# Kernel tuning notes

Measured on AMD Instinct MI355X. Metric: run time of the kernel, lower is better.

The kernel has to match this reference:

```python
import jax, jax.numpy as jnp
import numpy as np

N_NODES = 50000
N_EDGES = 800000
D = 128
N_GRAPHS = 64


def setup_inputs() -> dict:
    key = jax.random.key(0)
    ks = jax.random.split(key, 10)
    x = jax.random.normal(ks[0], (N_NODES, D), dtype=jnp.float32)
    edge_weight = jax.random.uniform(ks[1], (N_EDGES,), dtype=jnp.float32)
    W1 = jax.random.normal(ks[2], (D, D), dtype=jnp.float32) / np.sqrt(D)
    b1 = jax.random.normal(ks[3], (D,), dtype=jnp.float32) * 0.01
    W2 = jax.random.normal(ks[4], (D, D), dtype=jnp.float32) / np.sqrt(D)
    b2 = jax.random.normal(ks[5], (D,), dtype=jnp.float32) * 0.01
    Wh = jax.random.normal(ks[6], (D, 1), dtype=jnp.float32) / np.sqrt(D)
    bh = jax.random.normal(ks[7], (1,), dtype=jnp.float32) * 0.01
    edge_index = jax.random.randint(ks[8], (2, N_EDGES), 0, N_NODES, dtype=jnp.int64)
    batch = jnp.sort(jax.random.randint(ks[9], (N_NODES,), 0, N_GRAPHS, dtype=jnp.int64))
    return {"x": x, "edge_weight": edge_weight, "W1": W1, "b1": b1,
            "W2": W2, "b2": b2, "Wh": Wh, "bh": bh,
            "edge_index": edge_index, "batch": batch}


def reference(x, edge_weight, W1, b1, W2, b2, Wh, bh, edge_index, batch):
    N = x.shape[0]
    # --- GCN normalization with self-loops (computed once; shared by layers) ---
    row, col = edge_index[0], edge_index[1]
    loop = jnp.arange(N, dtype=edge_index.dtype)
    row2 = jnp.concatenate([row, loop])   # source nodes
    col2 = jnp.concatenate([col, loop])   # target nodes
    ew2 = jnp.concatenate([edge_weight, jnp.ones((N,), dtype=x.dtype)])
    deg = jax.ops.segment_sum(ew2, col2, num_segments=N)
    dinv = jnp.where(deg > 0, jax.lax.rsqrt(deg), 0.0)
    norm = dinv[row2] * ew2 * dinv[col2]  # [E+N]

    def gcn_conv(h, W, b):
        h = h @ W                                   # [N, D_out]
        msg = norm[:, None] * h[row2]               # gather + scale, [E+N, D_out]
        return jax.ops.segment_sum(msg, col2, num_segments=N) + b

    # dropout is identity in eval mode
    h = jax.nn.relu(gcn_conv(x, W1, b1))
    h = jax.nn.relu(gcn_conv(h, W2, b2))

    # --- global mean pool over graphs ---
    counts = jax.ops.segment_sum(jnp.ones((N,), dtype=h.dtype), batch, num_segments=N_GRAPHS)
    pooled = jax.ops.segment_sum(h, batch, num_segments=N_GRAPHS)
    pooled = pooled / jnp.maximum(counts, 1.0)[:, None]
    return pooled @ Wh + bh
```

## Files before the change

kernel.cpp:

```cpp
#include <hip/hip_runtime.h>
#include <hip/hip_bf16.h>
#include <hip/hip_fp16.h>
#include <hip/hip_fp8.h>

#define N_NODES  50000
#define N_EDGES  800000
#define D        128
#define N_GRAPHS 64
#define CAP      64
#define EW_SCALE 1048576.0f
#define NB_GEMM1 391
#define NB_FILL  3125
#define NB_AGG16 3125
#define PSTR     ((size_t)N_NODES * 64)

typedef _Float16 half8 __attribute__((ext_vector_type(8)));
typedef _Float16 half4 __attribute__((ext_vector_type(4)));
typedef float   float4v __attribute__((ext_vector_type(4)));
typedef float   f32x2   __attribute__((ext_vector_type(2)));

__device__ __forceinline__ float hu2f(unsigned short u) {
    __half_raw hr; hr.x = u;
    return __half2float(__half(hr));
}
__device__ __forceinline__ float fp8_f32(unsigned char u) {
    f32x2 v = __builtin_amdgcn_cvt_pk_f32_fp8((int)u, false);
    return v[0];
}
__device__ __forceinline__ unsigned char f32_fp8(float f) {
    __hip_fp8_e4m3 q(f);
    return (unsigned char)q.__x;
}
__device__ __forceinline__ void unpack_pd(unsigned long long p, int& n, float& dv) {
    int c = (int)(p >> 40);
    n = c < CAP ? c : CAP;
    dv = rsqrtf(1.0f + (float)(p & 0xFFFFFFFFFFULL) * (1.0f / EW_SCALE));
}

__global__ __launch_bounds__(256) void fused_gemm1_fill(const float* __restrict__ X,
                                                        const float* __restrict__ W,
                                                        unsigned char* __restrict__ Y8,
                                                        const int* __restrict__ ei,
                                                        const float* __restrict__ ew,
                                                        unsigned long long* __restrict__ packed,
                                                        unsigned int* __restrict__ bucket) {
    __shared__ _Float16 Xs[128][72];
    __shared__ _Float16 Wt[128][72];

    if (blockIdx.x >= NB_GEMM1) {
        int e = (blockIdx.x - NB_GEMM1) * 256 + threadIdx.x;
        if (e >= N_EDGES) return;
        int r = ei[e];
        int c = ei[N_EDGES + e];
        float w = ew[e];
        unsigned long long add = (1ULL << 40) | (unsigned long long)(unsigned)(w * EW_SCALE + 0.5f);
        unsigned long long old = atomicAdd(&packed[c], add);
        unsigned pos = (unsigned)(old >> 40);
        if (pos < CAP) {
            unsigned short wh = __half_as_ushort(__float2half_rn(w));
            bucket[(size_t)c * CAP + pos] = (unsigned)r | ((unsigned)wh << 16);
        }
        return;
    }

    const int tid  = threadIdx.x;
    const int row0 = blockIdx.x * 128;
    const int wv   = tid >> 6;
    const int lane = tid & 63;
    const int quad = lane >> 4;
    const int l16  = lane & 15;

    float4v acc[8][2] = {};

    for (int kt = 0; kt < 4; kt++) {
        const int kbase = kt * 32;
        {
            int r  = tid >> 1;
            int rr = row0 + r; if (rr >= N_NODES) rr = N_NODES - 1;
            int k0 = (tid & 1) * 16;
            const float4* src = (const float4*)(X + (size_t)rr * 128 + kbase + k0);
#pragma unroll
            for (int i = 0; i < 4; i++) {
                float4 v = src[i];
                half4 hv;
                hv[0] = (_Float16)v.x; hv[1] = (_Float16)v.y;
                hv[2] = (_Float16)v.z; hv[3] = (_Float16)v.w;
                *(half4*)(&Xs[r][k0 + i * 4]) = hv;
            }
        }
        {
            int k  = tid >> 3;
            int c0 = (tid & 7) * 16;
            const float4* src = (const float4*)(W + (size_t)(kbase + k) * 128 + c0);
#pragma unroll
            for (int i = 0; i < 4; i++) {
                float4 v = src[i];
                Wt[c0 + i * 4 + 0][k] = (_Float16)v.x;
                Wt[c0 + i * 4 + 1][k] = (_Float16)v.y;
                Wt[c0 + i * 4 + 2][k] = (_Float16)v.z;
                Wt[c0 + i * 4 + 3][k] = (_Float16)v.w;
            }
        }
        __syncthreads();

        half8 b0 = *(const half8*)(&Wt[wv * 32 + l16][quad * 8]);
        half8 b1f = *(const half8*)(&Wt[wv * 32 + 16 + l16][quad * 8]);
#pragma unroll
        for (int rt = 0; rt < 8; rt++) {
            half8 a = *(const half8*)(&Xs[rt * 16 + l16][quad * 8]);
            acc[rt][0] = __builtin_amdgcn_mfma_f32_16x16x32_f16(a, b0,  acc[rt][0], 0, 0, 0);
            acc[rt][1] = __builtin_amdgcn_mfma_f32_16x16x32_f16(a, b1f, acc[rt][1], 0, 0, 0);
        }
        __syncthreads();
    }
#pragma unroll
    for (int rt = 0; rt < 8; rt++)
#pragma unroll
        for (int ct = 0; ct < 2; ct++)
#pragma unroll
            for (int r = 0; r < 4; r++) {
                int row = row0 + rt * 16 + quad * 4 + r;
                int col = wv * 32 + ct * 16 + l16;
                if (row < N_NODES)
                    Y8[(size_t)(col >> 6) * PSTR + (size_t)row * 64 + (col & 63)] =
                        f32_fp8(acc[rt][ct][r]);
            }
}

__global__ __launch_bounds__(512) void agg1_gemm2_kernel(const unsigned char* __restrict__ x8in,
                                                         const unsigned long long* __restrict__ packed,
                                                         const unsigned int* __restrict__ bucket,
                                                         const float* __restrict__ b1,
                                                         const float* __restrict__ W2,
                                                         unsigned char* __restrict__ x2) {
    __shared__ _Float16 sh1[16][136];
    const int wv   = threadIdx.x >> 6;
    const int lane = threadIdx.x & 63;
    const int node0 = blockIdx.x * 16;

    const int nodeA = node0 + wv * 2;
    const int nodeB = nodeA + 1;
    int nA; float dvA; unpack_pd(packed[nodeA], nA, dvA);
    int nB; float dvB; unpack_pd(packed[nodeB], nB, dvB);

    unsigned pkA = 0u, pkB = 0u;
    if (lane < nA) {
        unsigned eh = bucket[(size_t)nodeA * CAP + lane];
        int src = eh & 0xFFFFu;
        int sn; float sdv; unpack_pd(packed[src], sn, sdv);
        float v = hu2f((unsigned short)(eh >> 16)) * sdv;
        pkA = (unsigned)src | ((unsigned)__half_as_ushort(__float2half_rn(v)) << 16);
    }
    if (lane < nB) {
        unsigned eh = bucket[(size_t)nodeB * CAP + lane];
        int src = eh & 0xFFFFu;
        int sn; float sdv; unpack_pd(packed[src], sn, sdv);
        float v = hu2f((unsigned short)(eh >> 16)) * sdv;
        pkB = (unsigned)src | ((unsigned)__half_as_ushort(__float2half_rn(v)) << 16);
    }
    int pkiA = (int)pkA, pkiB = (int)pkB;
    int nmax = nA > nB ? nA : nB;

    float hA[2], hB[2];
#pragma unroll
    for (int p = 0; p < 2; p++) {
        const unsigned char* pl = x8in + (size_t)p * PSTR;
        float aA = dvA * fp8_f32(pl[(size_t)nodeA * 64 + lane]);
        float aB = dvB * fp8_f32(pl[(size_t)nodeB * 64 + lane]);
        for (int i = 0; i < nmax; i += 8) {
            unsigned av[8], bv[8];
#pragma unroll
            for (int j = 0; j < 8; j++) {
                av[j] = (unsigned)__shfl(pkiA, i + j);
                bv[j] = (unsigned)__shfl(pkiB, i + j);
            }
            unsigned char mA[8], mB[8];
#pragma unroll
            for (int j = 0; j < 8; j++) mA[j] = pl[(size_t)(av[j] & 0xFFFFu) * 64 + lane];
#pragma unroll
            for (int j = 0; j < 8; j++) mB[j] = pl[(size_t)(bv[j] & 0xFFFFu) * 64 + lane];
#pragma unroll
            for (int j = 0; j < 8; j++)
                aA += hu2f((unsigned short)(av[j] >> 16)) * fp8_f32(mA[j]);
#pragma unroll
            for (int j = 0; j < 8; j++)
                aB += hu2f((unsigned short)(bv[j] >> 16)) * fp8_f32(mB[j]);
        }
        float bb = b1[p * 64 + lane];
        hA[p] = fmaxf(dvA * aA + bb, 0.0f);
        hB[p] = fmaxf(dvB * aB + bb, 0.0f);
    }

    sh1[wv * 2][lane]          = (_Float16)hA[0];
    sh1[wv * 2][64 + lane]     = (_Float16)hA[1];
    sh1[wv * 2 + 1][lane]      = (_Float16)hB[0];
    sh1[wv * 2 + 1][64 + lane] = (_Float16)hB[1];
    __syncthreads();

    const int quad = lane >> 4;
    const int l16  = lane & 15;
    float4v acc0 = {};
#pragma unroll
    for (int kc = 0; kc < 4; kc++) {
        const int k0 = kc * 32;
        half8 a = *(const half8*)(&sh1[l16][k0 + quad * 8]);
        const float* wp = W2 + (size_t)(k0 + quad * 8) * 128 + wv * 16 + l16;
        half8 b;
#pragma unroll
        for (int jj = 0; jj < 8; jj++) b[jj] = (_Float16)wp[jj * 128];
        acc0 = __builtin_amdgcn_mfma_f32_16x16x32_f16(a, b, acc0, 0, 0, 0);
    }
    const int col = wv * 16 + l16;
    unsigned char* x2p = x2 + (size_t)(col >> 6) * PSTR + (col & 63);
#pragma unroll
    for (int r = 0; r < 4; r++) {
        int row = node0 + quad * 4 + r;
        int rn; float s;
        unpack_pd(packed[row], rn, s);
        x2p[(size_t)row * 64] = f32_fp8(acc0[r] * s);
    }
}

__global__ __launch_bounds__(256) void agg_head_kernel(const unsigned char* __restrict__ x8,
                                                       const unsigned long long* __restrict__ packed,
                                                       const unsigned int* __restrict__ bucket,
                                                       const float* __restrict__ bias,
                                                       const float* __restrict__ Wh,
                                                       float* __restrict__ nodedot) {
    const int wv   = threadIdx.x >> 6;
    const int lane = threadIdx.x & 63;

    const int nodeA = blockIdx.x * 8 + wv * 2;
    const int nodeB = nodeA + 1;
    int nA; float dvA; unpack_pd(packed[nodeA], nA, dvA);
    int nB; float dvB; unpack_pd(packed[nodeB], nB, dvB);

    unsigned ehA = (lane < nA) ? bucket[(size_t)nodeA * CAP + lane] : 0u;
    unsigned ehB = (lane < nB) ? bucket[(size_t)nodeB * CAP + lane] : 0u;
    int eiA = (int)ehA, eiB = (int)ehB;
    int nmax = nA > nB ? nA : nB;

    float sA = 0.0f, sB = 0.0f;
#pragma unroll
    for (int p = 0; p < 2; p++) {
        const unsigned char* pl = x8 + (size_t)p * PSTR;
        float aA = fp8_f32(pl[(size_t)nodeA * 64 + lane]);
        float aB = fp8_f32(pl[(size_t)nodeB * 64 + lane]);
        for (int i = 0; i < nmax; i += 8) {
            unsigned av[8], bv[8];
#pragma unroll
            for (int j = 0; j < 8; j++) {
                av[j] = (unsigned)__shfl(eiA, i + j);
                bv[j] = (unsigned)__shfl(eiB, i + j);
            }
            unsigned char mA[8], mB[8];
#pragma unroll
            for (int j = 0; j < 8; j++) mA[j] = pl[(size_t)(av[j] & 0xFFFFu) * 64 + lane];
#pragma unroll
            for (int j = 0; j < 8; j++) mB[j] = pl[(size_t)(bv[j] & 0xFFFFu) * 64 + lane];
#pragma unroll
            for (int j = 0; j < 8; j++)
                aA += hu2f((unsigned short)(av[j] >> 16)) * fp8_f32(mA[j]);
#pragma unroll
            for (int j = 0; j < 8; j++)
                aB += hu2f((unsigned short)(bv[j] >> 16)) * fp8_f32(mB[j]);
        }
        float bb = bias[p * 64 + lane];
        float ww = Wh[p * 64 + lane];
        sA += fmaxf(dvA * aA + bb, 0.0f) * ww;
        sB += fmaxf(dvB * aB + bb, 0.0f) * ww;
    }

#pragma unroll
    for (int off = 32; off > 0; off >>= 1) {
        sA += __shfl_down(sA, off, 64);
        sB += __shfl_down(sB, off, 64);
    }
    if (lane == 0) {
        nodedot[nodeA] = sA;
        nodedot[nodeB] = sB;
    }
}

__global__ __launch_bounds__(256) void final2_kernel(const float* __restrict__ nodedot,
                                                     const int* __restrict__ batch,
                                                     const float* __restrict__ bh,
                                                     float* __restrict__ out) {
    __shared__ float red[256];
    int g = blockIdx.x;
    int lo = 0, hi = N_NODES;
    while (lo < hi) { int mid = (lo + hi) >> 1; if (batch[mid] < g) lo = mid + 1; else hi = mid; }
    int a = lo;
    hi = N_NODES;
    while (lo < hi) { int mid = (lo + hi) >> 1; if (batch[mid] < g + 1) lo = mid + 1; else hi = mid; }
    int b = lo;

    float s = 0.0f;
    for (int n = a + threadIdx.x; n < b; n += 256) s += nodedot[n];
    red[threadIdx.x] = s;
    __syncthreads();
#pragma unroll
    for (int off = 128; off > 0; off >>= 1) {
        if (threadIdx.x < off) red[threadIdx.x] += red[threadIdx.x + off];
        __syncthreads();
    }
    if (threadIdx.x == 0)
        out[g] = red[0] / fmaxf((float)(b - a), 1.0f) + bh[0];
}

extern "C" void kernel_launch(void* const* d_in, const int* in_sizes, int n_in,
                              void* d_out, int out_size, void* d_ws, size_t ws_size,
                              hipStream_t stream) {
    const float* x   = (const float*)d_in[0];
    const float* ew  = (const float*)d_in[1];
    const float* W1  = (const float*)d_in[2];
    const float* b1  = (const float*)d_in[3];
    const float* W2  = (const float*)d_in[4];
    const float* b2  = (const float*)d_in[5];
    const float* Wh  = (const float*)d_in[6];
    const float* bh  = (const float*)d_in[7];
    const int*   ei  = (const int*)d_in[8];
    const int*   bat = (const int*)d_in[9];
    float* out = (float*)d_out;

    char* ws = (char*)d_ws;
    unsigned char* bufA8 = (unsigned char*)ws;            ws += (size_t)N_NODES * D;
    unsigned char* bufB8 = (unsigned char*)ws;            ws += (size_t)N_NODES * D;
    ws += 128 - ((size_t)ws & 127);
    unsigned int* bucket = (unsigned int*)ws;             ws += (size_t)N_NODES * CAP * 4;
    unsigned long long* packed = (unsigned long long*)ws; ws += (size_t)N_NODES * 8;
    float*  nodedot = (float*)ws;                         ws += (size_t)N_NODES * 4;

    const int nb_agg8 = N_NODES / 8;

    hipMemsetAsync(packed, 0, (size_t)N_NODES * 8, stream);

    fused_gemm1_fill<<<NB_GEMM1 + NB_FILL, 256, 0, stream>>>(x, W1, bufA8, ei, ew, packed, bucket);

    agg1_gemm2_kernel<<<NB_AGG16, 512, 0, stream>>>(bufA8, packed, bucket, b1, W2, bufB8);

    agg_head_kernel<<<nb_agg8, 256, 0, stream>>>(bufB8, packed, bucket, b2, Wh, nodedot);

    final2_kernel<<<N_GRAPHS, 256, 0, stream>>>(nodedot, bat, bh, out);
}
```

Measured before the change: 231.4 us.

## Split aggregation kernels per feature plane and unfuse GEMM2 into tiled kernel

Both aggregation kernels now split the two 64-wide fp8 feature planes across separate blocks, doubling block count so that each block touches only one plane's gather footprint, which may improve L2 locality. The fused agg1+GEMM2 is split into an aggregation that writes fp16 H1 to global memory and a separate 128-row tiled MFMA GEMM. This removes the per-block reloading and conversion of W2 from fp32. It adds a 12.8MB fp16 round trip plus an extra launch, and the bucket and edge setup work is now duplicated per plane. Bucket reads use nontemporal loads, and the head partial sums are kept per plane and combined in the final kernel.

```diff
diff --git a/kernel.cpp b/kernel.cpp
--- a/kernel.cpp
+++ b/kernel.cpp
@@ -11,7 +11,6 @@
 #define EW_SCALE 1048576.0f
 #define NB_GEMM1 391
 #define NB_FILL  3125
-#define NB_AGG16 3125
 #define PSTR     ((size_t)N_NODES * 64)
 
 typedef _Float16 half8 __attribute__((ext_vector_type(8)));
@@ -127,16 +126,16 @@
             }
 }
 
-__global__ __launch_bounds__(512) void agg1_gemm2_kernel(const unsigned char* __restrict__ x8in,
+__global__ __launch_bounds__(512) void agg1_plane_kernel(const unsigned char* __restrict__ x8in,
                                                          const unsigned long long* __restrict__ packed,
                                                          const unsigned int* __restrict__ bucket,
                                                          const float* __restrict__ b1,
-                                                         const float* __restrict__ W2,
-                                                         unsigned char* __restrict__ x2) {
-    __shared__ _Float16 sh1[16][136];
+                                                         _Float16* __restrict__ h1out) {
+    const int p    = blockIdx.x & 1;
+    const int grp  = blockIdx.x >> 1;
     const int wv   = threadIdx.x >> 6;
     const int lane = threadIdx.x & 63;
-    const int node0 = blockIdx.x * 16;
+    const int node0 = grp * 16;
 
     const int nodeA = node0 + wv * 2;
     const int nodeB = nodeA + 1;
@@ -145,14 +144,14 @@
 
     unsigned pkA = 0u, pkB = 0u;
     if (lane < nA) {
-        unsigned eh = bucket[(size_t)nodeA * CAP + lane];
+        unsigned eh = __builtin_nontemporal_load(&bucket[(size_t)nodeA * CAP + lane]);
         int src = eh & 0xFFFFu;
         int sn; float sdv; unpack_pd(packed[src], sn, sdv);
         float v = hu2f((unsigned short)(eh >> 16)) * sdv;
         pkA = (unsigned)src | ((unsigned)__half_as_ushort(__float2half_rn(v)) << 16);
     }
     if (lane < nB) {
-        unsigned eh = bucket[(size_t)nodeB * CAP + lane];
+        unsigned eh = __builtin_nontemporal_load(&bucket[(size_t)nodeB * CAP + lane]);
         int src = eh & 0xFFFFu;
         int sn; float sdv; unpack_pd(packed[src], sn, sdv);
         float v = hu2f((unsigned short)(eh >> 16)) * sdv;
@@ -161,124 +160,160 @@
     int pkiA = (int)pkA, pkiB = (int)pkB;
     int nmax = nA > nB ? nA : nB;
 
-    float hA[2], hB[2];
-#pragma unroll
-    for (int p = 0; p < 2; p++) {
-        const unsigned char* pl = x8in + (size_t)p * PSTR;
-        float aA = dvA * fp8_f32(pl[(size_t)nodeA * 64 + lane]);
-        float aB = dvB * fp8_f32(pl[(size_t)nodeB * 64 + lane]);
-        for (int i = 0; i < nmax; i += 8) {
-            unsigned av[8], bv[8];
-#pragma unroll
-            for (int j = 0; j < 8; j++) {
-                av[j] = (unsigned)__shfl(pkiA, i + j);
-                bv[j] = (unsigned)__shfl(pkiB, i + j);
-            }
-            unsigned char mA[8], mB[8];
-#pragma unroll
-            for (int j = 0; j < 8; j++) mA[j] = pl[(size_t)(av[j] & 0xFFFFu) * 64 + lane];
-#pragma unroll
-            for (int j = 0; j < 8; j++) mB[j] = pl[(size_t)(bv[j] & 0xFFFFu) * 64 + lane];
-#pragma unroll
-            for (int j = 0; j < 8; j++)
-                aA += hu2f((unsigned short)(av[j] >> 16)) * fp8_f32(mA[j]);
-#pragma unroll
-            for (int j = 0; j < 8; j++)
-                aB += hu2f((unsigned short)(bv[j] >> 16)) * fp8_f32(mB[j]);
-        }
-        float bb = b1[p * 64 + lane];
-        hA[p] = fmaxf(dvA * aA + bb, 0.0f);
-        hB[p] = fmaxf(dvB * aB + bb, 0.0f);
-    }
-
-    sh1[wv * 2][lane]          = (_Float16)hA[0];
-    sh1[wv * 2][64 + lane]     = (_Float16)hA[1];
-    sh1[wv * 2 + 1][lane]      = (_Float16)hB[0];
-    sh1[wv * 2 + 1][64 + lane] = (_Float16)hB[1];
-    __syncthreads();
-
+    const unsigned char* pl = x8in + (size_t)p * PSTR;
+    float aA = dvA * fp8_f32(pl[(size_t)nodeA * 64 + lane]);
+    float aB = dvB * fp8_f32(pl[(size_t)nodeB * 64 + lane]);
+    for (int i = 0; i < nmax; i += 8) {
+        unsigned av[8], bv[8];
+#pragma unroll
+        for (int j = 0; j < 8; j++) {
+            av[j] = (unsigned)__shfl(pkiA, i + j);
+            bv[j] = (unsigned)__shfl(pkiB, i + j);
+        }
+        unsigned char mA[8], mB[8];
+#pragma unroll
+        for (int j = 0; j < 8; j++) mA[j] = pl[(size_t)(av[j] & 0xFFFFu) * 64 + lane];
+#pragma unroll
+        for (int j = 0; j < 8; j++) mB[j] = pl[(size_t)(bv[j] & 0xFFFFu) * 64 + lane];
+#pragma unroll
+        for (int j = 0; j < 8; j++)
+            aA += hu2f((unsigned short)(av[j] >> 16)) * fp8_f32(mA[j]);
+#pragma unroll
+        for (int j = 0; j < 8; j++)
+            aB += hu2f((unsigned short)(bv[j] >> 16)) * fp8_f32(mB[j]);
+    }
+
+    float bb = b1[p * 64 + lane];
+    _Float16 hA = (_Float16)fmaxf(dvA * aA + bb, 0.0f);
+    _Float16 hB = (_Float16)fmaxf(dvB * aB + bb, 0.0f);
+    __builtin_nontemporal_store(hA, &h1out[(size_t)nodeA * 128 + p * 64 + lane]);
+    __builtin_nontemporal_store(hB, &h1out[(size_t)nodeB * 128 + p * 64 + lane]);
+}
+
+__global__ __launch_bounds__(256) void gemm2_kernel(const _Float16* __restrict__ H1,
+                                                    const float* __restrict__ W,
+                                                    const unsigned long long* __restrict__ packed,
+                                                    unsigned char* __restrict__ Y8) {
+    __shared__ _Float16 Xs[128][72];
+    __shared__ _Float16 Wt[128][72];
+
+    const int tid  = threadIdx.x;
+    const int row0 = blockIdx.x * 128;
+    const int wv   = tid >> 6;
+    const int lane = tid & 63;
     const int quad = lane >> 4;
     const int l16  = lane & 15;
-    float4v acc0 = {};
-#pragma unroll
-    for (int kc = 0; kc < 4; kc++) {
-        const int k0 = kc * 32;
-        half8 a = *(const half8*)(&sh1[l16][k0 + quad * 8]);
-        const float* wp = W2 + (size_t)(k0 + quad * 8) * 128 + wv * 16 + l16;
-        half8 b;
-#pragma unroll
-        for (int jj = 0; jj < 8; jj++) b[jj] = (_Float16)wp[jj * 128];
-        acc0 = __builtin_amdgcn_mfma_f32_16x16x32_f16(a, b, acc0, 0, 0, 0);
-    }
-    const int col = wv * 16 + l16;
-    unsigned char* x2p = x2 + (size_t)(col >> 6) * PSTR + (col & 63);
-#pragma unroll
-    for (int r = 0; r < 4; r++) {
-        int row = node0 + quad * 4 + r;
-        int rn; float s;
-        unpack_pd(packed[row], rn, s);
-        x2p[(size_t)row * 64] = f32_fp8(acc0[r] * s);
-    }
-}
-
-__global__ __launch_bounds__(256) void agg_head_kernel(const unsigned char* __restrict__ x8,
-                                                       const unsigned long long* __restrict__ packed,
-                                                       const unsigned int* __restrict__ bucket,
-                                                       const float* __restrict__ bias,
-                                                       const float* __restrict__ Wh,
-                                                       float* __restrict__ nodedot) {
+
+    float4v acc[8][2] = {};
+
+    for (int kt = 0; kt < 4; kt++) {
+        const int kbase = kt * 32;
+        {
+            int r  = tid >> 1;
+            int rr = row0 + r; if (rr >= N_NODES) rr = N_NODES - 1;
+            int k0 = (tid & 1) * 16;
+            const half8* src = (const half8*)(H1 + (size_t)rr * 128 + kbase + k0);
+            *(half8*)(&Xs[r][k0])     = src[0];
+            *(half8*)(&Xs[r][k0 + 8]) = src[1];
+        }
+        {
+            int k  = tid >> 3;
+            int c0 = (tid & 7) * 16;
+            const float4* src = (const float4*)(W + (size_t)(kbase + k) * 128 + c0);
+#pragma unroll
+            for (int i = 0; i < 4; i++) {
+                float4 v = src[i];
+                Wt[c0 + i * 4 + 0][k] = (_Float16)v.x;
+                Wt[c0 + i * 4 + 1][k] = (_Float16)v.y;
+                Wt[c0 + i * 4 + 2][k] = (_Float16)v.z;
+                Wt[c0 + i * 4 + 3][k] = (_Float16)v.w;
+            }
+        }
+        __syncthreads();
+
+        half8 b0 = *(const half8*)(&Wt[wv * 32 + l16][quad * 8]);
+        half8 b1f = *(const half8*)(&Wt[wv * 32 + 16 + l16][quad * 8]);
+#pragma unroll
+        for (int rt = 0; rt < 8; rt++) {
+            half8 a = *(const half8*)(&Xs[rt * 16 + l16][quad * 8]);
+            acc[rt][0] = __builtin_amdgcn_mfma_f32_16x16x32_f16(a, b0,  acc[rt][0], 0, 0, 0);
+            acc[rt][1] = __builtin_amdgcn_mfma_f32_16x16x32_f16(a, b1f, acc[rt][1], 0, 0, 0);
+        }
+        __syncthreads();
+    }
+#pragma unroll
+    for (int rt = 0; rt < 8; rt++)
+#pragma unroll
+        for (int ct = 0; ct < 2; ct++)
+#pragma unroll
+            for (int r = 0; r < 4; r++) {
+                int row = row0 + rt * 16 + quad * 4 + r;
+                int col = wv * 32 + ct * 16 + l16;
+                if (row < N_NODES) {
+                    int rn; float s;
+                    unpack_pd(packed[row], rn, s);
+                    Y8[(size_t)(col >> 6) * PSTR + (size_t)row * 64 + (col & 63)] =
+                        f32_fp8(acc[rt][ct][r] * s);
+                }
+            }
+}
+
+__global__ __launch_bounds__(256) void agg_head_plane(const unsigned char* __restrict__ x8,
+                                                      const unsigned long long* __restrict__ packed,
+                                                      const unsigned int* __restrict__ bucket,
+                                                      const float* __restrict__ bias,
+                                                      const float* __restrict__ Wh,
+                                                      float* __restrict__ nodedot) {
+    const int p    = blockIdx.x & 1;
+    const int grp  = blockIdx.x >> 1;
     const int wv   = threadIdx.x >> 6;
     const int lane = threadIdx.x & 63;
 
-    const int nodeA = blockIdx.x * 8 + wv * 2;
+    const int nodeA = grp * 8 + wv * 2;
     const int nodeB = nodeA + 1;
     int nA; float dvA; unpack_pd(packed[nodeA], nA, dvA);
     int nB; float dvB; unpack_pd(packed[nodeB], nB, dvB);
 
-    unsigned ehA = (lane < nA) ? bucket[(size_t)nodeA * CAP + lane] : 0u;
-    unsigned ehB = (lane < nB) ? bucket[(size_t)nodeB * CAP + lane] : 0u;
+    unsigned ehA = (lane < nA) ? __builtin_nontemporal_load(&bucket[(size_t)nodeA * CAP + lane]) : 0u;
+    unsigned ehB = (lane < nB) ? __builtin_nontemporal_load(&bucket[(size_t)nodeB * CAP + lane]) : 0u;
     int eiA = (int)ehA, eiB = (int)ehB;
     int nmax = nA > nB ? nA : nB;
 
-    float sA = 0.0f, sB = 0.0f;
-#pragma unroll
-    for (int p = 0; p < 2; p++) {
-        const unsigned char* pl = x8 + (size_t)p * PSTR;
-        float aA = fp8_f32(pl[(size_t)nodeA * 64 + lane]);
-        float aB = fp8_f32(pl[(size_t)nodeB * 64 + lane]);
-        for (int i = 0; i < nmax; i += 8) {
-            unsigned av[8], bv[8];
-#pragma unroll
-            for (int j = 0; j < 8; j++) {
-                av[j] = (unsigned)__shfl(eiA, i + j);
-                bv[j] = (unsigned)__shfl(eiB, i + j);
-            }
-            unsigned char mA[8], mB[8];
-#pragma unroll
-            for (int j = 0; j < 8; j++) mA[j] = pl[(size_t)(av[j] & 0xFFFFu) * 64 + lane];
-#pragma unroll
-            for (int j = 0; j < 8; j++) mB[j] = pl[(size_t)(bv[j] & 0xFFFFu) * 64 + lane];
-#pragma unroll
-            for (int j = 0; j < 8; j++)
-                aA += hu2f((unsigned short)(av[j] >> 16)) * fp8_f32(mA[j]);
-#pragma unroll
-            for (int j = 0; j < 8; j++)
-                aB += hu2f((unsigned short)(bv[j] >> 16)) * fp8_f32(mB[j]);
-        }
-        float bb = bias[p * 64 + lane];
-        float ww = Wh[p * 64 + lane];
-        sA += fmaxf(dvA * aA + bb, 0.0f) * ww;
-        sB += fmaxf(dvB * aB + bb, 0.0f) * ww;
-    }
-
+    const unsigned char* pl = x8 + (size_t)p * PSTR;
+    float aA = fp8_f32(pl[(size_t)nodeA * 64 + lane]);
+    float aB = fp8_f32(pl[(size_t)nodeB * 64 + lane]);
+    for (int i = 0; i < nmax; i += 8) {
+        unsigned av[8], bv[8];
+#pragma unroll
+        for (int j = 0; j < 8; j++) {
+            av[j] = (unsigned)__shfl(eiA, i + j);
+            bv[j] = (unsigned)__shfl(eiB, i + j);
+        }
+        unsigned char mA[8], mB[8];
+#pragma unroll
+        for (int j = 0; j < 8; j++) mA[j] = pl[(size_t)(av[j] & 0xFFFFu) * 64 + lane];
+#pragma unroll
+        for (int j = 0; j < 8; j++) mB[j] = pl[(size_t)(bv[j] & 0xFFFFu) * 64 + lane];
+#pragma unroll
+        for (int j = 0; j < 8; j++)
+            aA += hu2f((unsigned short)(av[j] >> 16)) * fp8_f32(mA[j]);
+#pragma unroll
+        for (int j = 0; j < 8; j++)
+            aB += hu2f((unsigned short)(bv[j] >> 16)) * fp8_f32(mB[j]);
+    }
+
+    float bb = bias[p * 64 + lane];
+    float ww = Wh[p * 64 + lane];
+    float sA = fmaxf(dvA * aA + bb, 0.0f) * ww;
+    float sB = fmaxf(dvB * aB + bb, 0.0f) * ww;
 #pragma unroll
     for (int off = 32; off > 0; off >>= 1) {
         sA += __shfl_down(sA, off, 64);
         sB += __shfl_down(sB, off, 64);
     }
     if (lane == 0) {
-        nodedot[nodeA] = sA;
-        nodedot[nodeB] = sB;
+        nodedot[(size_t)p * N_NODES + nodeA] = sA;
+        nodedot[(size_t)p * N_NODES + nodeB] = sB;
     }
 }
 
@@ -296,7 +331,8 @@
     int b = lo;
 
     float s = 0.0f;
-    for (int n = a + threadIdx.x; n < b; n += 256) s += nodedot[n];
+    for (int n = a + threadIdx.x; n < b; n += 256)
+        s += nodedot[n] + nodedot[(size_t)N_NODES + n];
     red[threadIdx.x] = s;
     __syncthreads();
 #pragma unroll
@@ -329,17 +365,18 @@
     ws += 128 - ((size_t)ws & 127);
     unsigned int* bucket = (unsigned int*)ws;             ws += (size_t)N_NODES * CAP * 4;
     unsigned long long* packed = (unsigned long long*)ws; ws += (size_t)N_NODES * 8;
-    float*  nodedot = (float*)ws;                         ws += (size_t)N_NODES * 4;
-
-    const int nb_agg8 = N_NODES / 8;
+    float*  nodedot = (float*)ws;                         ws += (size_t)N_NODES * 2 * 4;
+    _Float16* h1buf = (_Float16*)ws;                      ws += (size_t)N_NODES * D * 2;
 
     hipMemsetAsync(packed, 0, (size_t)N_NODES * 8, stream);
 
     fused_gemm1_fill<<<NB_GEMM1 + NB_FILL, 256, 0, stream>>>(x, W1, bufA8, ei, ew, packed, bucket);
 
-    agg1_gemm2_kernel<<<NB_AGG16, 512, 0, stream>>>(bufA8, packed, bucket, b1, W2, bufB8);
-
-    agg_head_kernel<<<nb_agg8, 256, 0, stream>>>(bufB8, packed, bucket, b2, Wh, nodedot);
+    agg1_plane_kernel<<<2 * 3125, 512, 0, stream>>>(bufA8, packed, bucket, b1, h1buf);
+
+    gemm2_kernel<<<NB_GEMM1, 256, 0, stream>>>(h1buf, W2, packed, bufB8);
+
+    agg_head_plane<<<2 * 6250, 256, 0, stream>>>(bufB8, packed, bucket, b2, Wh, nodedot);
 
     final2_kernel<<<N_GRAPHS, 256, 0, stream>>>(nodedot, bat, bh, out);
 }
```

New measurement: 246.5 us. 6.5% more time.

## Switch FP8 features to row-major and gather 8-byte chunks per lane

Applied to the files above, without the earlier changes.

Feature buffers move from two 64-column planes to a row-major 128-byte-per-node layout. The aggregation loops now have each 16-lane group fetch one full neighbor row as 8-byte loads, so four neighbors are handled per wave at once. The per-feature partial sums are then combined across groups with xor shuffles. This cuts the number of byte-sized gather instructions and the two plane passes, at the cost of more registers (8 accumulators per node) and extra cross-lane reductions. Bucket reads are also marked nontemporal.

```diff
diff --git a/kernel.cpp b/kernel.cpp
--- a/kernel.cpp
+++ b/kernel.cpp
@@ -12,7 +12,6 @@
 #define NB_GEMM1 391
 #define NB_FILL  3125
 #define NB_AGG16 3125
-#define PSTR     ((size_t)N_NODES * 64)
 
 typedef _Float16 half8 __attribute__((ext_vector_type(8)));
 typedef _Float16 half4 __attribute__((ext_vector_type(4)));
@@ -22,10 +21,6 @@
 __device__ __forceinline__ float hu2f(unsigned short u) {
     __half_raw hr; hr.x = u;
     return __half2float(__half(hr));
-}
-__device__ __forceinline__ float fp8_f32(unsigned char u) {
-    f32x2 v = __builtin_amdgcn_cvt_pk_f32_fp8((int)u, false);
-    return v[0];
 }
 __device__ __forceinline__ unsigned char f32_fp8(float f) {
     __hip_fp8_e4m3 q(f);
@@ -122,8 +117,7 @@
                 int row = row0 + rt * 16 + quad * 4 + r;
                 int col = wv * 32 + ct * 16 + l16;
                 if (row < N_NODES)
-                    Y8[(size_t)(col >> 6) * PSTR + (size_t)row * 64 + (col & 63)] =
-                        f32_fp8(acc[rt][ct][r]);
+                    Y8[(size_t)row * 128 + col] = f32_fp8(acc[rt][ct][r]);
             }
 }
 
@@ -136,6 +130,8 @@
     __shared__ _Float16 sh1[16][136];
     const int wv   = threadIdx.x >> 6;
     const int lane = threadIdx.x & 63;
+    const int g    = lane >> 4;
+    const int fl   = lane & 15;
     const int node0 = blockIdx.x * 16;
 
     const int nodeA = node0 + wv * 2;
@@ -145,14 +141,14 @@
 
     unsigned pkA = 0u, pkB = 0u;
     if (lane < nA) {
-        unsigned eh = bucket[(size_t)nodeA * CAP + lane];
+        unsigned eh = __builtin_nontemporal_load(&bucket[(size_t)nodeA * CAP + lane]);
         int src = eh & 0xFFFFu;
         int sn; float sdv; unpack_pd(packed[src], sn, sdv);
         float v = hu2f((unsigned short)(eh >> 16)) * sdv;
         pkA = (unsigned)src | ((unsigned)__half_as_ushort(__float2half_rn(v)) << 16);
     }
     if (lane < nB) {
-        unsigned eh = bucket[(size_t)nodeB * CAP + lane];
+        unsigned eh = __builtin_nontemporal_load(&bucket[(size_t)nodeB * CAP + lane]);
         int src = eh & 0xFFFFu;
         int sn; float sdv; unpack_pd(packed[src], sn, sdv);
         float v = hu2f((unsigned short)(eh >> 16)) * sdv;
@@ -161,40 +157,86 @@
     int pkiA = (int)pkA, pkiB = (int)pkB;
     int nmax = nA > nB ? nA : nB;
 
-    float hA[2], hB[2];
-#pragma unroll
-    for (int p = 0; p < 2; p++) {
-        const unsigned char* pl = x8in + (size_t)p * PSTR;
-        float aA = dvA * fp8_f32(pl[(size_t)nodeA * 64 + lane]);
-        float aB = dvB * fp8_f32(pl[(size_t)nodeB * 64 + lane]);
-        for (int i = 0; i < nmax; i += 8) {
-            unsigned av[8], bv[8];
-#pragma unroll
-            for (int j = 0; j < 8; j++) {
-                av[j] = (unsigned)__shfl(pkiA, i + j);
-                bv[j] = (unsigned)__shfl(pkiB, i + j);
-            }
-            unsigned char mA[8], mB[8];
-#pragma unroll
-            for (int j = 0; j < 8; j++) mA[j] = pl[(size_t)(av[j] & 0xFFFFu) * 64 + lane];
-#pragma unroll
-            for (int j = 0; j < 8; j++) mB[j] = pl[(size_t)(bv[j] & 0xFFFFu) * 64 + lane];
-#pragma unroll
-            for (int j = 0; j < 8; j++)
-                aA += hu2f((unsigned short)(av[j] >> 16)) * fp8_f32(mA[j]);
-#pragma unroll
-            for (int j = 0; j < 8; j++)
-                aB += hu2f((unsigned short)(bv[j] >> 16)) * fp8_f32(mB[j]);
-        }
-        float bb = b1[p * 64 + lane];
-        hA[p] = fmaxf(dvA * aA + bb, 0.0f);
-        hB[p] = fmaxf(dvB * aB + bb, 0.0f);
-    }
-
-    sh1[wv * 2][lane]          = (_Float16)hA[0];
-    sh1[wv * 2][64 + lane]     = (_Float16)hA[1];
-    sh1[wv * 2 + 1][lane]      = (_Float16)hB[0];
-    sh1[wv * 2 + 1][64 + lane] = (_Float16)hB[1];
+    const unsigned char* base = x8in + fl * 8;
+
+    float aA[8] = {}, aB[8] = {};
+    for (int i = 0; i < nmax; i += 8) {
+        unsigned hA0 = (unsigned)__shfl(pkiA, i + g);
+        unsigned hA1 = (unsigned)__shfl(pkiA, i + 4 + g);
+        unsigned hB0 = (unsigned)__shfl(pkiB, i + g);
+        unsigned hB1 = (unsigned)__shfl(pkiB, i + 4 + g);
+        uint2 dA0 = *(const uint2*)(base + (size_t)(hA0 & 0xFFFFu) * 128);
+        uint2 dA1 = *(const uint2*)(base + (size_t)(hA1 & 0xFFFFu) * 128);
+        uint2 dB0 = *(const uint2*)(base + (size_t)(hB0 & 0xFFFFu) * 128);
+        uint2 dB1 = *(const uint2*)(base + (size_t)(hB1 & 0xFFFFu) * 128);
+        float vA0 = hu2f((unsigned short)(hA0 >> 16));
+        float vA1 = hu2f((unsigned short)(hA1 >> 16));
+        float vB0 = hu2f((unsigned short)(hB0 >> 16));
+        float vB1 = hu2f((unsigned short)(hB1 >> 16));
+#pragma unroll
+        for (int d = 0; d < 2; d++) {
+            unsigned wA0 = d ? dA0.y : dA0.x;
+            unsigned wA1 = d ? dA1.y : dA1.x;
+            unsigned wB0 = d ? dB0.y : dB0.x;
+            unsigned wB1 = d ? dB1.y : dB1.x;
+            f32x2 A0lo = __builtin_amdgcn_cvt_pk_f32_fp8((int)wA0, false);
+            f32x2 A0hi = __builtin_amdgcn_cvt_pk_f32_fp8((int)wA0, true);
+            f32x2 A1lo = __builtin_amdgcn_cvt_pk_f32_fp8((int)wA1, false);
+            f32x2 A1hi = __builtin_amdgcn_cvt_pk_f32_fp8((int)wA1, true);
+            f32x2 B0lo = __builtin_amdgcn_cvt_pk_f32_fp8((int)wB0, false);
+            f32x2 B0hi = __builtin_amdgcn_cvt_pk_f32_fp8((int)wB0, true);
+            f32x2 B1lo = __builtin_amdgcn_cvt_pk_f32_fp8((int)wB1, false);
+            f32x2 B1hi = __builtin_amdgcn_cvt_pk_f32_fp8((int)wB1, true);
+            aA[d*4+0] += vA0 * A0lo[0] + vA1 * A1lo[0];
+            aA[d*4+1] += vA0 * A0lo[1] + vA1 * A1lo[1];
+            aA[d*4+2] += vA0 * A0hi[0] + vA1 * A1hi[0];
+            aA[d*4+3] += vA0 * A0hi[1] + vA1 * A1hi[1];
+            aB[d*4+0] += vB0 * B0lo[0] + vB1 * B1lo[0];
+            aB[d*4+1] += vB0 * B0lo[1] + vB1 * B1lo[1];
+            aB[d*4+2] += vB0 * B0hi[0] + vB1 * B1hi[0];
+            aB[d*4+3] += vB0 * B0hi[1] + vB1 * B1hi[1];
+        }
+    }
+
+#pragma unroll
+    for (int k = 0; k < 8; k++) {
+        aA[k] += __shfl_xor(aA[k], 16, 64);
+        aA[k] += __shfl_xor(aA[k], 32, 64);
+        aB[k] += __shfl_xor(aB[k], 16, 64);
+        aB[k] += __shfl_xor(aB[k], 32, 64);
+    }
+
+    {
+        uint2 dsA = *(const uint2*)(base + (size_t)nodeA * 128);
+        uint2 dsB = *(const uint2*)(base + (size_t)nodeB * 128);
+#pragma unroll
+        for (int d = 0; d < 2; d++) {
+            unsigned wA = d ? dsA.y : dsA.x;
+            unsigned wB = d ? dsB.y : dsB.x;
+            f32x2 Alo = __builtin_amdgcn_cvt_pk_f32_fp8((int)wA, false);
+            f32x2 Ahi = __builtin_amdgcn_cvt_pk_f32_fp8((int)wA, true);
+            f32x2 Blo = __builtin_amdgcn_cvt_pk_f32_fp8((int)wB, false);
+            f32x2 Bhi = __builtin_amdgcn_cvt_pk_f32_fp8((int)wB, true);
+            aA[d*4+0] += dvA * Alo[0]; aA[d*4+1] += dvA * Alo[1];
+            aA[d*4+2] += dvA * Ahi[0]; aA[d*4+3] += dvA * Ahi[1];
+            aB[d*4+0] += dvB * Blo[0]; aB[d*4+1] += dvB * Blo[1];
+            aB[d*4+2] += dvB * Bhi[0]; aB[d*4+3] += dvB * Bhi[1];
+        }
+    }
+
+    if (g == 0) {
+        float4 bb0 = ((const float4*)b1)[fl * 2];
+        float4 bb1 = ((const float4*)b1)[fl * 2 + 1];
+        float bb[8] = {bb0.x, bb0.y, bb0.z, bb0.w, bb1.x, bb1.y, bb1.z, bb1.w};
+        half8 hvA, hvB;
+#pragma unroll
+        for (int k = 0; k < 8; k++) {
+            hvA[k] = (_Float16)fmaxf(dvA * aA[k] + bb[k], 0.0f);
+            hvB[k] = (_Float16)fmaxf(dvB * aB[k] + bb[k], 0.0f);
+        }
+        *(half8*)(&sh1[wv * 2][fl * 8])     = hvA;
+        *(half8*)(&sh1[wv * 2 + 1][fl * 8]) = hvB;
+    }
     __syncthreads();
 
     const int quad = lane >> 4;
@@ -210,14 +252,12 @@
         for (int jj = 0; jj < 8; jj++) b[jj] = (_Float16)wp[jj * 128];
         acc0 = __builtin_amdgcn_mfma_f32_16x16x32_f16(a, b, acc0, 0, 0, 0);
     }
-    const int col = wv * 16 + l16;
-    unsigned char* x2p = x2 + (size_t)(col >> 6) * PSTR + (col & 63);
 #pragma unroll
     for (int r = 0; r < 4; r++) {
         int row = node0 + quad * 4 + r;
         int rn; float s;
         unpack_pd(packed[row], rn, s);
-        x2p[(size_t)row * 64] = f32_fp8(acc0[r] * s);
+        x2[(size_t)row * 128 + wv * 16 + l16] = f32_fp8(acc0[r] * s);
     }
 }
 
@@ -229,52 +269,102 @@
                                                        float* __restrict__ nodedot) {
     const int wv   = threadIdx.x >> 6;
     const int lane = threadIdx.x & 63;
+    const int g    = lane >> 4;
+    const int fl   = lane & 15;
 
     const int nodeA = blockIdx.x * 8 + wv * 2;
     const int nodeB = nodeA + 1;
     int nA; float dvA; unpack_pd(packed[nodeA], nA, dvA);
     int nB; float dvB; unpack_pd(packed[nodeB], nB, dvB);
 
-    unsigned ehA = (lane < nA) ? bucket[(size_t)nodeA * CAP + lane] : 0u;
-    unsigned ehB = (lane < nB) ? bucket[(size_t)nodeB * CAP + lane] : 0u;
+    unsigned ehA = (lane < nA) ? __builtin_nontemporal_load(&bucket[(size_t)nodeA * CAP + lane]) : 0u;
+    unsigned ehB = (lane < nB) ? __builtin_nontemporal_load(&bucket[(size_t)nodeB * CAP + lane]) : 0u;
     int eiA = (int)ehA, eiB = (int)ehB;
     int nmax = nA > nB ? nA : nB;
 
+    const unsigned char* base = x8 + fl * 8;
+
+    float aA[8] = {}, aB[8] = {};
+    for (int i = 0; i < nmax; i += 8) {
+        unsigned hA0 = (unsigned)__shfl(eiA, i + g);
+        unsigned hA1 = (unsigned)__shfl(eiA, i + 4 + g);
+        unsigned hB0 = (unsigned)__shfl(eiB, i + g);
+        unsigned hB1 = (unsigned)__shfl(eiB, i + 4 + g);
+        uint2 dA0 = *(const uint2*)(base + (size_t)(hA0 & 0xFFFFu) * 128);
+        uint2 dA1 = *(const uint2*)(base + (size_t)(hA1 & 0xFFFFu) * 128);
+        uint2 dB0 = *(const uint2*)(base + (size_t)(hB0 & 0xFFFFu) * 128);
+        uint2 dB1 = *(const uint2*)(base + (size_t)(hB1 & 0xFFFFu) * 128);
+        float vA0 = hu2f((unsigned short)(hA0 >> 16));
+        float vA1 = hu2f((unsigned short)(hA1 >> 16));
+        float vB0 = hu2f((unsigned short)(hB0 >> 16));
+        float vB1 = hu2f((unsigned short)(hB1 >> 16));
+#pragma unroll
+        for (int d = 0; d < 2; d++) {
+            unsigned wA0 = d ? dA0.y : dA0.x;
+            unsigned wA1 = d ? dA1.y : dA1.x;
+            unsigned wB0 = d ? dB0.y : dB0.x;
+            unsigned wB1 = d ? dB1.y : dB1.x;
+            f32x2 A0lo = __builtin_amdgcn_cvt_pk_f32_fp8((int)wA0, false);
+            f32x2 A0hi = __builtin_amdgcn_cvt_pk_f32_fp8((int)wA0, true);
+            f32x2 A1lo = __builtin_amdgcn_cvt_pk_f32_fp8((int)wA1, false);
+            f32x2 A1hi = __builtin_amdgcn_cvt_pk_f32_fp8((int)wA1, true);
+            f32x2 B0lo = __builtin_amdgcn_cvt_pk_f32_fp8((int)wB0, false);
+            f32x2 B0hi = __builtin_amdgcn_cvt_pk_f32_fp8((int)wB0, true);
+            f32x2 B1lo = __builtin_amdgcn_cvt_pk_f32_fp8((int)wB1, false);
+            f32x2 B1hi = __builtin_amdgcn_cvt_pk_f32_fp8((int)wB1, true);
+            aA[d*4+0] += vA0 * A0lo[0] + vA1 * A1lo[0];
+            aA[d*4+1] += vA0 * A0lo[1] + vA1 * A1lo[1];
+            aA[d*4+2] += vA0 * A0hi[0] + vA1 * A1hi[0];
+            aA[d*4+3] += vA0 * A0hi[1] + vA1 * A1hi[1];
+            aB[d*4+0] += vB0 * B0lo[0] + vB1 * B1lo[0];
+            aB[d*4+1] += vB0 * B0lo[1] + vB1 * B1lo[1];
+            aB[d*4+2] += vB0 * B0hi[0] + vB1 * B1hi[0];
+            aB[d*4+3] += vB0 * B0hi[1] + vB1 * B1hi[1];
+        }
+    }
+
+#pragma unroll
+    for (int k = 0; k < 8; k++) {
+        aA[k] += __shfl_xor(aA[k], 16, 64);
+        aA[k] += __shfl_xor(aA[k], 32, 64);
+        aB[k] += __shfl_xor(aB[k], 16, 64);
+        aB[k] += __shfl_xor(aB[k], 32, 64);
+    }
+
+    {
+        uint2 dsA = *(const uint2*)(base + (size_t)nodeA * 128);
+        uint2 dsB = *(const uint2*)(base + (size_t)nodeB * 128);
+#pragma unroll
+        for (int d = 0; d < 2; d++) {
+            unsigned wA = d ? dsA.y : dsA.x;
+            unsigned wB = d ? dsB.y : dsB.x;
+            f32x2 Alo = __builtin_amdgcn_cvt_pk_f32_fp8((int)wA, false);
+            f32x2 Ahi = __builtin_amdgcn_cvt_pk_f32_fp8((int)wA, true);
+            f32x2 Blo = __builtin_amdgcn_cvt_pk_f32_fp8((int)wB, false);
+            f32x2 Bhi = __builtin_amdgcn_cvt_pk_f32_fp8((int)wB, true);
+            aA[d*4+0] += Alo[0]; aA[d*4+1] += Alo[1];
+            aA[d*4+2] += Ahi[0]; aA[d*4+3] += Ahi[1];
+            aB[d*4+0] += Blo[0]; aB[d*4+1] += Blo[1];
+            aB[d*4+2] += Bhi[0]; aB[d*4+3] += Bhi[1];
+        }
+    }
+
+    float4 bb0 = ((const float4*)bias)[fl * 2];
+    float4 bb1 = ((const float4*)bias)[fl * 2 + 1];
+    float4 wh0 = ((const float4*)Wh)[fl * 2];
+    float4 wh1 = ((const float4*)Wh)[fl * 2 + 1];
+    float bb[8] = {bb0.x, bb0.y, bb0.z, bb0.w, bb1.x, bb1.y, bb1.z, bb1.w};
+    float ww[8] = {wh0.x, wh0.y, wh0.z, wh0.w, wh1.x, wh1.y, wh1.z, wh1.w};
     float sA = 0.0f, sB = 0.0f;
 #pragma unroll
-    for (int p = 0; p < 2; p++) {
-        const unsigned char* pl = x8 + (size_t)p * PSTR;
-        float aA = fp8_f32(pl[(size_t)nodeA * 64 + lane]);
-        float aB = fp8_f32(pl[(size_t)nodeB * 64 + lane]);
-        for (int i = 0; i < nmax; i += 8) {
-            unsigned av[8], bv[8];
-#pragma unroll
-            for (int j = 0; j < 8; j++) {
-                av[j] = (unsigned)__shfl(eiA, i + j);
-                bv[j] = (unsigned)__shfl(eiB, i + j);
-            }
-            unsigned char mA[8], mB[8];
-#pragma unroll
-            for (int j = 0; j < 8; j++) mA[j] = pl[(size_t)(av[j] & 0xFFFFu) * 64 + lane];
-#pragma unroll
-            for (int j = 0; j < 8; j++) mB[j] = pl[(size_t)(bv[j] & 0xFFFFu) * 64 + lane];
-#pragma unroll
-            for (int j = 0; j < 8; j++)
-                aA += hu2f((unsigned short)(av[j] >> 16)) * fp8_f32(mA[j]);
-#pragma unroll
-            for (int j = 0; j < 8; j++)
-                aB += hu2f((unsigned short)(bv[j] >> 16)) * fp8_f32(mB[j]);
-        }
-        float bb = bias[p * 64 + lane];
-        float ww = Wh[p * 64 + lane];
-        sA += fmaxf(dvA * aA + bb, 0.0f) * ww;
-        sB += fmaxf(dvB * aB + bb, 0.0f) * ww;
-    }
-
-#pragma unroll
-    for (int off = 32; off > 0; off >>= 1) {
-        sA += __shfl_down(sA, off, 64);
-        sB += __shfl_down(sB, off, 64);
+    for (int k = 0; k < 8; k++) {
+        sA += fmaxf(dvA * aA[k] + bb[k], 0.0f) * ww[k];
+        sB += fmaxf(dvB * aB[k] + bb[k], 0.0f) * ww[k];
+    }
+#pragma unroll
+    for (int off = 8; off > 0; off >>= 1) {
+        sA += __shfl_xor(sA, off, 64);
+        sB += __shfl_xor(sB, off, 64);
     }
     if (lane == 0) {
         nodedot[nodeA] = sA;
@@ -331,15 +421,13 @@
     unsigned long long* packed = (unsigned long long*)ws; ws += (size_t)N_NODES * 8;
     float*  nodedot = (float*)ws;                         ws += (size_t)N_NODES * 4;
 
-    const int nb_agg8 = N_NODES / 8;
-
     hipMemsetAsync(packed, 0, (size_t)N_NODES * 8, stream);
 
     fused_gemm1_fill<<<NB_GEMM1 + NB_FILL, 256, 0, stream>>>(x, W1, bufA8, ei, ew, packed, bucket);
 
     agg1_gemm2_kernel<<<NB_AGG16, 512, 0, stream>>>(bufA8, packed, bucket, b1, W2, bufB8);
 
-    agg_head_kernel<<<nb_agg8, 256, 0, stream>>>(bufB8, packed, bucket, b2, Wh, nodedot);
+    agg_head_kernel<<<6250, 256, 0, stream>>>(bufB8, packed, bucket, b2, Wh, nodedot);
 
     final2_kernel<<<N_GRAPHS, 256, 0, stream>>>(nodedot, bat, bh, out);
 }
```

Result: faster. 209.4 us (-9.5%).
